# Kernel tuning notes

Measured on AMD Instinct MI355X. Metric: run time of the kernel, lower is better.

Reference implementation:

```python
import jax, jax.numpy as jnp
import numpy as np

DIM = 1024
HEADS = 16
HEAD_DIM = DIM // HEADS
B, S = 2, 2048


def setup_inputs() -> dict:
    key = jax.random.key(0)
    ks = jax.random.split(key, 10)
    sc = lambda fan_in: 1.0 / np.sqrt(fan_in)
    return {
        "x": jax.random.normal(ks[0], (B, S, 1), dtype=jnp.float32),
        "w_in": jax.random.uniform(ks[1], (1, DIM), jnp.float32, -1.0, 1.0),
        "b_in": jax.random.uniform(ks[2], (DIM,), jnp.float32, -1.0, 1.0),
        "wq": jax.random.uniform(ks[3], (DIM, DIM), jnp.float32, -sc(DIM), sc(DIM)),
        "wk": jax.random.uniform(ks[4], (DIM, DIM), jnp.float32, -sc(DIM), sc(DIM)),
        "wv": jax.random.uniform(ks[5], (DIM, DIM), jnp.float32, -sc(DIM), sc(DIM)),
        "wo": jax.random.uniform(ks[6], (DIM, DIM), jnp.float32, -sc(DIM), sc(DIM)),
        "bo": jax.random.uniform(ks[7], (DIM,), jnp.float32, -sc(DIM), sc(DIM)),
        "wf": jax.random.uniform(ks[8], (DIM, 1), jnp.float32, -sc(DIM), sc(DIM)),
        "bf": jax.random.uniform(ks[9], (1,), jnp.float32, -sc(DIM), sc(DIM)),
    }


def reference(x, w_in, b_in, wq, wk, wv, wo, bo, wf, bf):
    b, s, _ = x.shape
    scale = HEAD_DIM ** -0.5
    h = x @ w_in + b_in                      # [b, s, dim]
    q = (h @ wq).reshape(b, s, HEADS, HEAD_DIM)
    k = (h @ wk).reshape(b, s, HEADS, HEAD_DIM)
    v = (h @ wv).reshape(b, s, HEADS, HEAD_DIM)
    scores = jnp.einsum("bqhd,bkhd->bhqk", q, k) * scale  # [b, h, s, s]
    causal = jnp.triu(jnp.ones((s, s), dtype=bool), k=1)
    scores = jnp.where(causal, -jnp.inf, scores)
    attn = jax.nn.softmax(scores, axis=-1)   # dropout is identity in eval
    out = jnp.einsum("bhqk,bkhd->bqhd", attn, v).reshape(b, s, DIM)
    out = out @ wo + bo
    out = out @ wf + bf                      # [b, s, 1]
    return jnp.transpose(out, (0, 2, 1))     # [b, 1, s]
```

## Files before the change

kernel.cpp:

```cpp
#include <hip/hip_runtime.h>

#define DIM 1024
#define HEADS 16
#define BATCH 2
#define SEQ 2048
#define NCHUNK 64
#define NTERM 32

#define WS_U    5120
#define WS_A    6144
#define WS_C    6160
#define WS_G    6176
#define WS_C0H  6192
#define WS_PART 8192
#define WS_T    344064

__global__ __launch_bounds__(256) void k1_weights(
        const float* __restrict__ x,
        const float* __restrict__ w_in, const float* __restrict__ b_in,
        const float* __restrict__ wq,   const float* __restrict__ wk,
        const float* __restrict__ wv,   const float* __restrict__ wo,
        const float* __restrict__ wf,   float* __restrict__ ws) {
    const int bid = blockIdx.x;
    const int tid = threadIdx.x;
    if (bid < NCHUNK) {
        const int j0 = bid * 16;
        float4 qa = {0,0,0,0}, qb = {0,0,0,0}, ka = {0,0,0,0};
        float4 va = {0,0,0,0}, vb = {0,0,0,0};
        #pragma unroll
        for (int j = j0; j < j0 + 16; ++j) {
            const float wi = w_in[j], bi = b_in[j];
            const float4 cq = ((const float4*)(wq + j * DIM))[tid];
            const float4 ck = ((const float4*)(wk + j * DIM))[tid];
            const float4 cv = ((const float4*)(wv + j * DIM))[tid];
            qa.x += wi * cq.x; qa.y += wi * cq.y; qa.z += wi * cq.z; qa.w += wi * cq.w;
            qb.x += bi * cq.x; qb.y += bi * cq.y; qb.z += bi * cq.z; qb.w += bi * cq.w;
            ka.x += wi * ck.x; ka.y += wi * ck.y; ka.z += wi * ck.z; ka.w += wi * ck.w;
            va.x += wi * cv.x; va.y += wi * cv.y; va.z += wi * cv.z; va.w += wi * cv.w;
            vb.x += bi * cv.x; vb.y += bi * cv.y; vb.z += bi * cv.z; vb.w += bi * cv.w;
        }
        float4* base = (float4*)(ws + WS_PART + bid * 5 * DIM);
        base[tid]           = qa;
        base[256 + tid]     = qb;
        base[2 * 256 + tid] = ka;
        base[3 * 256 + tid] = va;
        base[4 * 256 + tid] = vb;
    } else if (bid < 320) {
        const int wave = tid >> 6, lane = tid & 63;
        const int row = (bid - NCHUNK) * 4 + wave;
        const float4* wo4 = (const float4*)(wo + row * DIM);
        const float4* wf4 = (const float4*)wf;
        float s = 0.f;
        #pragma unroll
        for (int e = lane; e < 256; e += 64) {
            const float4 a = wo4[e], b = wf4[e];
            s += a.x * b.x + a.y * b.y + a.z * b.z + a.w * b.w;
        }
        #pragma unroll
        for (int off = 32; off; off >>= 1) s += __shfl_down(s, off);
        if (lane == 0) ws[WS_U + row] = s;
    } else {
        const int sb = bid - 320;
        const int b = sb >> 5, n = sb & 31;
        const float* xb = x + b * SEQ;
        const float4 xa = ((const float4*)xb)[2 * tid];
        const float4 xc = ((const float4*)xb)[2 * tid + 1];
        float xv[8] = {xa.x, xa.y, xa.z, xa.w, xc.x, xc.y, xc.z, xc.w};
        float pw[8];
        #pragma unroll
        for (int e = 0; e < 8; ++e) pw[e] = 1.f;
        float f = 1.f;
        for (int i = 1; i <= n; ++i) {
            f *= (float)i;
            #pragma unroll
            for (int e = 0; e < 8; ++e) pw[e] *= xv[e];
        }
        const float rf = 1.0f / f;
        float p[8];
        float s = 0.f;
        #pragma unroll
        for (int e = 0; e < 8; ++e) { s += pw[e] * rf; p[e] = s; }
        const int lane = tid & 63, wv = tid >> 6;
        float incl = s;
        #pragma unroll
        for (int off = 1; off < 64; off <<= 1) {
            const float v = __shfl_up(incl, off);
            if (lane >= off) incl += v;
        }
        __shared__ float wsum[4];
        if (lane == 63) wsum[wv] = incl;
        __syncthreads();
        float base = incl - s;
        if (wv > 0) base += wsum[0];
        if (wv > 1) base += wsum[1];
        if (wv > 2) base += wsum[2];
        float* Trow = ws + WS_T + (b * NTERM + n) * SEQ;
        ((float4*)Trow)[2 * tid]     = make_float4(base + p[0], base + p[1], base + p[2], base + p[3]);
        ((float4*)Trow)[2 * tid + 1] = make_float4(base + p[4], base + p[5], base + p[6], base + p[7]);
    }
}

__global__ __launch_bounds__(256) void k2_combine(
        const float* __restrict__ bo, const float* __restrict__ wf,
        const float* __restrict__ bf, float* __restrict__ ws) {
    const int h = blockIdx.x;
    const int tid = threadIdx.x;
    const int c4 = tid >> 6, dl = tid & 63;
    const int d = h * 64 + dl;
    float qa = 0.f, qb = 0.f, ka = 0.f, va = 0.f, vb = 0.f;
    for (int c = c4; c < NCHUNK; c += 4) {
        const float* base = ws + WS_PART + c * 5 * DIM + d;
        qa += base[0];
        qb += base[DIM];
        ka += base[2 * DIM];
        va += base[3 * DIM];
        vb += base[4 * DIM];
    }
    __shared__ float red5[4][5][64];
    red5[c4][0][dl] = qa;
    red5[c4][1][dl] = qb;
    red5[c4][2][dl] = ka;
    red5[c4][3][dl] = va;
    red5[c4][4][dl] = vb;
    __syncthreads();
    if (tid < 64) {
        const float fqa = red5[0][0][tid] + red5[1][0][tid] + red5[2][0][tid] + red5[3][0][tid];
        const float fqb = red5[0][1][tid] + red5[1][1][tid] + red5[2][1][tid] + red5[3][1][tid];
        const float fka = red5[0][2][tid] + red5[1][2][tid] + red5[2][2][tid] + red5[3][2][tid];
        const float fva = red5[0][3][tid] + red5[1][3][tid] + red5[2][3][tid] + red5[3][3][tid];
        const float fvb = red5[0][4][tid] + red5[1][4][tid] + red5[2][4][tid] + red5[3][4][tid];
        const int dd = h * 64 + tid;
        const float u = ws[WS_U + dd];
        float pA = fqa * fka;
        float pC = fqb * fka;
        float pG = fva * u;
        float pc = fvb * u + bo[dd] * wf[dd];
        #pragma unroll
        for (int off = 32; off; off >>= 1) {
            pA += __shfl_down(pA, off);
            pC += __shfl_down(pC, off);
            pG += __shfl_down(pG, off);
            pc += __shfl_down(pc, off);
        }
        if (tid == 0) {
            ws[WS_A + h]   = pA;
            ws[WS_C + h]   = pC;
            ws[WS_G + h]   = pG;
            ws[WS_C0H + h] = pc + (h == 0 ? bf[0] : 0.f);
        }
    }
}

__global__ __launch_bounds__(256) void k3_eval(
        const float* __restrict__ x, const float* __restrict__ ws,
        float* __restrict__ out) {
    const int g = blockIdx.x * 256 + threadIdx.x;
    const int h = g & 15;
    const int q = (g >> 4) & (SEQ - 1);
    const int b = g >> 15;
    const float xq = x[b * SEQ + q];
    const float al = 0.125f * (ws[WS_A + h] * xq + ws[WS_C + h]);
    const float* T = ws + WS_T + b * NTERM * SEQ + q;
    float tr[NTERM];
    #pragma unroll
    for (int n = 0; n < NTERM; ++n) tr[n] = T[n * SEQ];
    float den = tr[31];
    float num = 31.f * tr[31];
    #pragma unroll
    for (int j = 30; j >= 1; --j) {
        den = den * al + tr[j];
        num = num * al + (float)j * tr[j];
    }
    den = den * al + tr[0];
    float r = ws[WS_G + h] * (num / den);
    r += __shfl_down(r, 8);
    r += __shfl_down(r, 4);
    r += __shfl_down(r, 2);
    r += __shfl_down(r, 1);
    if (h == 0) {
        float c0 = 0.f;
        #pragma unroll
        for (int i = 0; i < HEADS; ++i) c0 += ws[WS_C0H + i];
        out[b * SEQ + q] = c0 + r;
    }
}

extern "C" void kernel_launch(void* const* d_in, const int* in_sizes, int n_in,
                              void* d_out, int out_size, void* d_ws, size_t ws_size,
                              hipStream_t stream) {
    const float* x    = (const float*)d_in[0];
    const float* w_in = (const float*)d_in[1];
    const float* b_in = (const float*)d_in[2];
    const float* wq   = (const float*)d_in[3];
    const float* wk   = (const float*)d_in[4];
    const float* wv   = (const float*)d_in[5];
    const float* wo   = (const float*)d_in[6];
    const float* bo   = (const float*)d_in[7];
    const float* wf   = (const float*)d_in[8];
    const float* bf   = (const float*)d_in[9];
    float* out = (float*)d_out;
    float* ws  = (float*)d_ws;

    k1_weights<<<384, 256, 0, stream>>>(x, w_in, b_in, wq, wk, wv, wo, wf, ws);
    k2_combine<<<HEADS, 256, 0, stream>>>(bo, wf, bf, ws);
    k3_eval<<<256, 256, 0, stream>>>(x, ws, out);
}
```

Before: 19.61 us.

## Merge combine into eval kernel and reduce weight projections in-block

The weight-projection stage now reduces each column chunk inside its block through shared memory and writes only two partial halves instead of 64 chunk partials. The separate combine kernel is removed, and every eval block recomputes the per-head scalars (A, C, G and the constant term) from those two halves. This drops one launch and a serial 16-block reduction stage. In exchange, all 256 eval blocks repeat the small combine work, and the wo·wf blocks now handle 16 rows each.

Result: faster. 16.15 us (-17.6%).

```diff
diff --git a/kernel.cpp b/kernel.cpp
--- a/kernel.cpp
+++ b/kernel.cpp
@@ -4,16 +4,12 @@
 #define HEADS 16
 #define BATCH 2
 #define SEQ 2048
-#define NCHUNK 64
 #define NTERM 32
 
-#define WS_U    5120
-#define WS_A    6144
-#define WS_C    6160
-#define WS_G    6176
-#define WS_C0H  6192
-#define WS_PART 8192
-#define WS_T    344064
+#define WS_P0   0
+#define WS_P1   5120
+#define WS_U    10240
+#define WS_T    16384
 
 __global__ __launch_bounds__(256) void k1_weights(
         const float* __restrict__ x,
@@ -23,44 +19,72 @@
         const float* __restrict__ wf,   float* __restrict__ ws) {
     const int bid = blockIdx.x;
     const int tid = threadIdx.x;
-    if (bid < NCHUNK) {
-        const int j0 = bid * 16;
-        float4 qa = {0,0,0,0}, qb = {0,0,0,0}, ka = {0,0,0,0};
-        float4 va = {0,0,0,0}, vb = {0,0,0,0};
-        #pragma unroll
-        for (int j = j0; j < j0 + 16; ++j) {
-            const float wi = w_in[j], bi = b_in[j];
-            const float4 cq = ((const float4*)(wq + j * DIM))[tid];
-            const float4 ck = ((const float4*)(wk + j * DIM))[tid];
-            const float4 cv = ((const float4*)(wv + j * DIM))[tid];
-            qa.x += wi * cq.x; qa.y += wi * cq.y; qa.z += wi * cq.z; qa.w += wi * cq.w;
-            qb.x += bi * cq.x; qb.y += bi * cq.y; qb.z += bi * cq.z; qb.w += bi * cq.w;
-            ka.x += wi * ck.x; ka.y += wi * ck.y; ka.z += wi * ck.z; ka.w += wi * ck.w;
-            va.x += wi * cv.x; va.y += wi * cv.y; va.z += wi * cv.z; va.w += wi * cv.w;
-            vb.x += bi * cv.x; vb.y += bi * cv.y; vb.z += bi * cv.z; vb.w += bi * cv.w;
-        }
-        float4* base = (float4*)(ws + WS_PART + bid * 5 * DIM);
-        base[tid]           = qa;
-        base[256 + tid]     = qb;
-        base[2 * 256 + tid] = ka;
-        base[3 * 256 + tid] = va;
-        base[4 * 256 + tid] = vb;
-    } else if (bid < 320) {
+    if (bid < 192) {
+        const int m  = bid >> 6;
+        const int r  = bid & 63;
+        const int jh = r & 1;
+        const int d0 = (r >> 1) * 32;
+        const int dl = tid & 7;
+        const int jg = tid >> 3;
+        const int j0 = jh * 512 + jg * 16;
+        const float* Wm = (m == 0) ? wq : (m == 1) ? wk : wv;
+        float4 a1 = {0, 0, 0, 0}, a2 = {0, 0, 0, 0};
+        #pragma unroll
+        for (int i = 0; i < 16; ++i) {
+            const int j = j0 + i;
+            const float4 v = *reinterpret_cast<const float4*>(Wm + j * DIM + d0 + 4 * dl);
+            const float wi = w_in[j];
+            a1.x += wi * v.x; a1.y += wi * v.y; a1.z += wi * v.z; a1.w += wi * v.w;
+            if (m != 1) {
+                const float bi = b_in[j];
+                a2.x += bi * v.x; a2.y += bi * v.y; a2.z += bi * v.z; a2.w += bi * v.w;
+            }
+        }
+        __shared__ float sh1[32][33], sh2[32][33];
+        sh1[jg][4 * dl + 0] = a1.x;
+        sh1[jg][4 * dl + 1] = a1.y;
+        sh1[jg][4 * dl + 2] = a1.z;
+        sh1[jg][4 * dl + 3] = a1.w;
+        if (m != 1) {
+            sh2[jg][4 * dl + 0] = a2.x;
+            sh2[jg][4 * dl + 1] = a2.y;
+            sh2[jg][4 * dl + 2] = a2.z;
+            sh2[jg][4 * dl + 3] = a2.w;
+        }
+        __syncthreads();
+        if (tid < 32) {
+            float f1 = 0.f, f2 = 0.f;
+            #pragma unroll
+            for (int g = 0; g < 32; ++g) {
+                f1 += sh1[g][tid];
+                if (m != 1) f2 += sh2[g][tid];
+            }
+            const int base = jh ? WS_P1 : WS_P0;
+            const int d = d0 + tid;
+            if (m == 0)      { ws[base + d] = f1; ws[base + 1024 + d] = f2; }
+            else if (m == 1) { ws[base + 2048 + d] = f1; }
+            else             { ws[base + 3072 + d] = f1; ws[base + 4096 + d] = f2; }
+        }
+    } else if (bid < 256) {
         const int wave = tid >> 6, lane = tid & 63;
-        const int row = (bid - NCHUNK) * 4 + wave;
-        const float4* wo4 = (const float4*)(wo + row * DIM);
-        const float4* wf4 = (const float4*)wf;
-        float s = 0.f;
-        #pragma unroll
-        for (int e = lane; e < 256; e += 64) {
-            const float4 a = wo4[e], b = wf4[e];
-            s += a.x * b.x + a.y * b.y + a.z * b.z + a.w * b.w;
-        }
-        #pragma unroll
-        for (int off = 32; off; off >>= 1) s += __shfl_down(s, off);
-        if (lane == 0) ws[WS_U + row] = s;
+        const int rb = bid - 192;
+        #pragma unroll
+        for (int rr = 0; rr < 4; ++rr) {
+            const int row = rb * 16 + wave * 4 + rr;
+            const float4* wo4 = reinterpret_cast<const float4*>(wo + row * DIM);
+            const float4* wf4 = reinterpret_cast<const float4*>(wf);
+            float s = 0.f;
+            #pragma unroll
+            for (int e = lane; e < 256; e += 64) {
+                const float4 a = wo4[e], b = wf4[e];
+                s += a.x * b.x + a.y * b.y + a.z * b.z + a.w * b.w;
+            }
+            #pragma unroll
+            for (int off = 32; off; off >>= 1) s += __shfl_down(s, off);
+            if (lane == 0) ws[WS_U + row] = s;
+        }
     } else {
-        const int sb = bid - 320;
+        const int sb = bid - 256;
         const int b = sb >> 5, n = sb & 31;
         const float* xb = x + b * SEQ;
         const float4 xa = ((const float4*)xb)[2 * tid];
@@ -100,66 +124,55 @@
     }
 }
 
-__global__ __launch_bounds__(256) void k2_combine(
-        const float* __restrict__ bo, const float* __restrict__ wf,
-        const float* __restrict__ bf, float* __restrict__ ws) {
-    const int h = blockIdx.x;
+__global__ __launch_bounds__(256) void k2_eval(
+        const float* __restrict__ x,  const float* __restrict__ bo,
+        const float* __restrict__ wf, const float* __restrict__ bf,
+        const float* __restrict__ ws, float* __restrict__ out) {
     const int tid = threadIdx.x;
-    const int c4 = tid >> 6, dl = tid & 63;
-    const int d = h * 64 + dl;
-    float qa = 0.f, qb = 0.f, ka = 0.f, va = 0.f, vb = 0.f;
-    for (int c = c4; c < NCHUNK; c += 4) {
-        const float* base = ws + WS_PART + c * 5 * DIM + d;
-        qa += base[0];
-        qb += base[DIM];
-        ka += base[2 * DIM];
-        va += base[3 * DIM];
-        vb += base[4 * DIM];
-    }
-    __shared__ float red5[4][5][64];
-    red5[c4][0][dl] = qa;
-    red5[c4][1][dl] = qb;
-    red5[c4][2][dl] = ka;
-    red5[c4][3][dl] = va;
-    red5[c4][4][dl] = vb;
-    __syncthreads();
-    if (tid < 64) {
-        const float fqa = red5[0][0][tid] + red5[1][0][tid] + red5[2][0][tid] + red5[3][0][tid];
-        const float fqb = red5[0][1][tid] + red5[1][1][tid] + red5[2][1][tid] + red5[3][1][tid];
-        const float fka = red5[0][2][tid] + red5[1][2][tid] + red5[2][2][tid] + red5[3][2][tid];
-        const float fva = red5[0][3][tid] + red5[1][3][tid] + red5[2][3][tid] + red5[3][3][tid];
-        const float fvb = red5[0][4][tid] + red5[1][4][tid] + red5[2][4][tid] + red5[3][4][tid];
-        const int dd = h * 64 + tid;
-        const float u = ws[WS_U + dd];
-        float pA = fqa * fka;
-        float pC = fqb * fka;
-        float pG = fva * u;
-        float pc = fvb * u + bo[dd] * wf[dd];
+    const int wave = tid >> 6, lane = tid & 63;
+
+    __shared__ float sA[HEADS], sC[HEADS], sG[HEADS];
+    __shared__ float c0p[4];
+
+    #pragma unroll
+    for (int hh = 0; hh < 4; ++hh) {
+        const int h = wave * 4 + hh;
+        const int d = h * 64 + lane;
+        const float qa = ws[WS_P0 + d]        + ws[WS_P1 + d];
+        const float qb = ws[WS_P0 + 1024 + d] + ws[WS_P1 + 1024 + d];
+        const float ka = ws[WS_P0 + 2048 + d] + ws[WS_P1 + 2048 + d];
+        const float va = ws[WS_P0 + 3072 + d] + ws[WS_P1 + 3072 + d];
+        const float u  = ws[WS_U + d];
+        float pA = qa * ka, pC = qb * ka, pG = va * u;
         #pragma unroll
         for (int off = 32; off; off >>= 1) {
             pA += __shfl_down(pA, off);
             pC += __shfl_down(pC, off);
             pG += __shfl_down(pG, off);
-            pc += __shfl_down(pc, off);
-        }
-        if (tid == 0) {
-            ws[WS_A + h]   = pA;
-            ws[WS_C + h]   = pC;
-            ws[WS_G + h]   = pG;
-            ws[WS_C0H + h] = pc + (h == 0 ? bf[0] : 0.f);
-        }
-    }
-}
-
-__global__ __launch_bounds__(256) void k3_eval(
-        const float* __restrict__ x, const float* __restrict__ ws,
-        float* __restrict__ out) {
-    const int g = blockIdx.x * 256 + threadIdx.x;
+        }
+        if (lane == 0) { sA[h] = pA; sC[h] = pC; sG[h] = pG; }
+    }
+    {
+        float s = 0.f;
+        #pragma unroll
+        for (int t = 0; t < 4; ++t) {
+            const int d = wave * 256 + t * 64 + lane;
+            const float vb = ws[WS_P0 + 4096 + d] + ws[WS_P1 + 4096 + d];
+            s += vb * ws[WS_U + d] + bo[d] * wf[d];
+        }
+        #pragma unroll
+        for (int off = 32; off; off >>= 1) s += __shfl_down(s, off);
+        if (lane == 0) c0p[wave] = s;
+    }
+    __syncthreads();
+    const float c0 = c0p[0] + c0p[1] + c0p[2] + c0p[3] + bf[0];
+
+    const int g = blockIdx.x * 256 + tid;
     const int h = g & 15;
     const int q = (g >> 4) & (SEQ - 1);
     const int b = g >> 15;
     const float xq = x[b * SEQ + q];
-    const float al = 0.125f * (ws[WS_A + h] * xq + ws[WS_C + h]);
+    const float al = 0.125f * (sA[h] * xq + sC[h]);
     const float* T = ws + WS_T + b * NTERM * SEQ + q;
     float tr[NTERM];
     #pragma unroll
@@ -172,17 +185,12 @@
         num = num * al + (float)j * tr[j];
     }
     den = den * al + tr[0];
-    float r = ws[WS_G + h] * (num / den);
+    float r = sG[h] * (num / den);
     r += __shfl_down(r, 8);
     r += __shfl_down(r, 4);
     r += __shfl_down(r, 2);
     r += __shfl_down(r, 1);
-    if (h == 0) {
-        float c0 = 0.f;
-        #pragma unroll
-        for (int i = 0; i < HEADS; ++i) c0 += ws[WS_C0H + i];
-        out[b * SEQ + q] = c0 + r;
-    }
+    if (h == 0) out[b * SEQ + q] = c0 + r;
 }
 
 extern "C" void kernel_launch(void* const* d_in, const int* in_sizes, int n_in,
@@ -201,7 +209,6 @@
     float* out = (float*)d_out;
     float* ws  = (float*)d_ws;
 
-    k1_weights<<<384, 256, 0, stream>>>(x, w_in, b_in, wq, wk, wv, wo, wf, ws);
-    k2_combine<<<HEADS, 256, 0, stream>>>(bo, wf, bf, ws);
-    k3_eval<<<256, 256, 0, stream>>>(x, ws, out);
+    k1_weights<<<320, 256, 0, stream>>>(x, w_in, b_in, wq, wk, wv, wo, wf, ws);
+    k2_eval<<<256, 256, 0, stream>>>(x, bo, wf, bf, ws, out);
 }
```
